# Kernel tuning notes

Hardware: AMD Instinct MI355X
Metric: run time of the kernel (lower is better)

Reference implementation:

```python
import jax, jax.numpy as jnp
import numpy as np

N_NODES = 32768
N_EDGES = 524288
IN_F = 256
OUT_F = 128
NB = 4


def setup_inputs() -> dict:
    key = jax.random.key(0)
    ks = jax.random.split(key, 12)
    s_in = 1.0 / np.sqrt(IN_F)
    s_out = 1.0 / np.sqrt(OUT_F)
    s_cat = 1.0 / np.sqrt(OUT_F * NB)
    return {
        "x": jax.random.normal(ks[0], (N_NODES, IN_F), dtype=jnp.float32),
        "edge_index": jax.random.randint(ks[1], (2, N_EDGES), 0, N_NODES, dtype=jnp.int64),
        "Wb": jax.random.uniform(ks[2], (NB, IN_F, OUT_F), jnp.float32, -s_in, s_in),
        "bb": jax.random.uniform(ks[3], (NB, OUT_F), jnp.float32, -s_in, s_in),
        "W1": jax.random.uniform(ks[4], (NB, OUT_F, OUT_F), jnp.float32, -s_out, s_out),
        "b1": jax.random.uniform(ks[5], (NB, OUT_F), jnp.float32, -s_out, s_out),
        "W2": jax.random.uniform(ks[6], (NB, OUT_F, OUT_F), jnp.float32, -s_out, s_out),
        "b2": jax.random.uniform(ks[7], (NB, OUT_F), jnp.float32, -s_out, s_out),
        "branch_gates": jnp.ones((NB,), dtype=jnp.float32),
        "temperature": jnp.asarray(1.0, dtype=jnp.float32),
        "Wo": jax.random.uniform(ks[8], (OUT_F * NB, OUT_F), jnp.float32, -s_cat, s_cat),
        "bo": jax.random.uniform(ks[9], (OUT_F,), jnp.float32, -s_cat, s_cat),
    }


def _scatter_mean_step(h, row, col, inv_deg):
    # gather per-edge source features, mean-reduce onto destination nodes
    sums = jax.ops.segment_sum(h[row], col, num_segments=N_NODES)
    return sums * inv_deg


def reference(x, edge_index, Wb, bb, W1, b1, W2, b2, branch_gates, temperature, Wo, bo):
    row, col = edge_index[0], edge_index[1]
    deg = jax.ops.segment_sum(jnp.ones((N_EDGES,), x.dtype), col, num_segments=N_NODES)
    inv_deg = (1.0 / jnp.maximum(deg, 1.0))[:, None]  # empty segments -> 0 (scatter_mean semantics)

    gates = jax.nn.softmax(branch_gates / temperature)

    branch_outputs = []
    for i in range(NB):
        h = x @ Wb[i] + bb[i]                   # [N, OUT_F]
        for _ in range(i):                       # scale = scales[i % 4] = i
            h = _scatter_mean_step(h, row, col, inv_deg)
        h = jax.nn.relu(h @ W1[i] + b1[i]) @ W2[i] + b2[i]
        branch_outputs.append(h * gates[i])

    concat = jnp.concatenate(branch_outputs, axis=1)  # [N, NB*OUT_F]
    return concat @ Wo + bo
```

## Files before the change

kernel.cpp:

```cpp
#include <hip/hip_runtime.h>
#include <math.h>

#define N_NODES 32768
#define N_EDGES 524288
#define IN_F    256
#define OUT_F   128
#define NB      4
#define STRIDE  96

#define NE_BLK   256
#define CONV_BLK 1024
#define GX_BLK   2048
#define GEMM_BLK (N_NODES / 128)
#define M_BLK    (N_NODES / 256)

typedef __attribute__((ext_vector_type(8))) short bf16x8;
typedef __attribute__((ext_vector_type(4))) float f32x4;
typedef __attribute__((ext_vector_type(4))) ushort u16x4;

__device__ __forceinline__ ushort f2b(float f) {
    uint u = __float_as_uint(f);
    return (ushort)((u + 0x7fffu + ((u >> 16) & 1u)) >> 16);
}
__device__ __forceinline__ float b2f_lo(uint v) { return __uint_as_float(v << 16); }
__device__ __forceinline__ float b2f_hi(uint v) { return __uint_as_float(v & 0xffff0000u); }

__device__ __forceinline__ float softmax_gate(const float* bg, const float* temp, int i) {
    float T = temp[0];
    float mx = fmaxf(fmaxf(bg[0], bg[1]), fmaxf(bg[2], bg[3]));
    float e0 = expf((bg[0] - mx) / T), e1 = expf((bg[1] - mx) / T);
    float e2 = expf((bg[2] - mx) / T), e3 = expf((bg[3] - mx) / T);
    float s = e0 + e1 + e2 + e3;
    float ei = (i == 0) ? e0 : (i == 1) ? e1 : (i == 2) ? e2 : e3;
    return ei / s;
}

__device__ __forceinline__ int detect_i32(const int* __restrict__ ei, int* sflag) {
    if (threadIdx.x < 64) {
        unsigned long long b = __ballot(ei[2 * threadIdx.x + 1] != 0);
        if (threadIdx.x == 0) *sflag = (b != 0ull) ? 1 : 0;
    }
    __syncthreads();
    return *sflag;
}

__global__ __launch_bounds__(256) void fill_all_kernel(
    const int* __restrict__ ei, int* __restrict__ cursor, int* __restrict__ srcs,
    const float* __restrict__ x, ushort* __restrict__ xb,
    const float* __restrict__ Wb, const float* __restrict__ W1,
    const float* __restrict__ W2, const float* __restrict__ Wo,
    const float* __restrict__ bb, const float* __restrict__ b2,
    const float* __restrict__ bo, const float* __restrict__ bg,
    const float* __restrict__ temp,
    ushort* __restrict__ WcT, ushort* __restrict__ WzT,
    float* __restrict__ u, float* __restrict__ cvec) {
    __shared__ float smem[16 * 128];
    __shared__ int sflag;
    int b = blockIdx.x;
    int tid = threadIdx.x;
    if (b < NE_BLK) {
        int i32 = detect_i32(ei, &sflag);
#pragma unroll
        for (int it = 0; it < 8; it++) {
            int e = b * 2048 + it * 256 + tid;
            int r, c;
            if (i32 == 0) {
                r = __builtin_nontemporal_load(ei + 2 * e);
                c = __builtin_nontemporal_load(ei + 2 * (N_EDGES + e));
            } else {
                r = __builtin_nontemporal_load(ei + e);
                c = __builtin_nontemporal_load(ei + N_EDGES + e);
            }
            int slot = atomicAdd(&cursor[c], 1);
            if (slot < STRIDE) srcs[(size_t)c * STRIDE + slot] = r;
        }
        return;
    }
    b -= NE_BLK;
    if (b < CONV_BLK) {
#pragma unroll
        for (int it = 0; it < 8; it++) {
            int idx = b * 2048 + it * 256 + tid;
            f32x4 v = __builtin_nontemporal_load((const f32x4*)x + idx);
            u16x4 o;
            o.x = f2b(v.x); o.y = f2b(v.y); o.z = f2b(v.z); o.w = f2b(v.w);
            *((u16x4*)xb + idx) = o;
        }
        return;
    }
    b -= CONV_BLK;
    int f = tid & 127, rh = tid >> 7;
    if (b < 64) {
        int i = b >> 4, k0 = (b & 15) * 16;
#pragma unroll
        for (int rr = 0; rr < 8; rr++)
            smem[(rh * 8 + rr) * 128 + f] = Wb[((size_t)i * IN_F + k0 + rh * 8 + rr) * OUT_F + f];
        __syncthreads();
        float acc[8] = {};
        const float* W1i = W1 + (size_t)i * OUT_F * OUT_F;
        for (int j = 0; j < OUT_F; j++) {
            float w1 = W1i[j * OUT_F + f];
#pragma unroll
            for (int rr = 0; rr < 8; rr++) acc[rr] += smem[(rh * 8 + rr) * 128 + j] * w1;
        }
        ushort tmp[8];
#pragma unroll
        for (int rr = 0; rr < 8; rr++) tmp[rr] = f2b(acc[rr]);
        *(uint4*)(WcT + ((size_t)i * OUT_F + f) * IN_F + k0 + rh * 8) = *(uint4*)tmp;
    } else if (b < 96) {
        int id = b - 64;
        int i = id >> 3, j0 = (id & 7) * 16;
#pragma unroll
        for (int rr = 0; rr < 8; rr++)
            smem[(rh * 8 + rr) * 128 + f] = W2[((size_t)i * OUT_F + j0 + rh * 8 + rr) * OUT_F + f];
        __syncthreads();
        float acc[8] = {};
        for (int l = 0; l < OUT_F; l++) {
            float wo = Wo[((size_t)i * OUT_F + l) * OUT_F + f];
#pragma unroll
            for (int rr = 0; rr < 8; rr++) acc[rr] += smem[(rh * 8 + rr) * 128 + l] * wo;
        }
        float g = softmax_gate(bg, temp, i);
        ushort tmp[8];
#pragma unroll
        for (int rr = 0; rr < 8; rr++) tmp[rr] = f2b(g * acc[rr]);
        *(uint4*)(WzT + (size_t)f * (NB * OUT_F) + i * OUT_F + j0 + rh * 8) = *(uint4*)tmp;
    } else {
        int id = b - 96;
        int jc = rh;
        if (id < NB) {
            int i = id;
            float partial = 0.f;
            for (int j = jc * 64; j < jc * 64 + 64; j++)
                partial += bb[i * OUT_F + j] * W1[((size_t)i * OUT_F + j) * OUT_F + f];
            smem[jc * 128 + f] = partial;
            __syncthreads();
            if (jc == 0) u[i * OUT_F + f] = smem[f] + smem[128 + f];
        } else {
            int i = id - NB;
            float partial = 0.f;
            for (int j = jc * 64; j < jc * 64 + 64; j++)
                partial += b2[i * OUT_F + j] * Wo[((size_t)i * OUT_F + j) * OUT_F + f];
            smem[jc * 128 + f] = partial;
            __syncthreads();
            if (jc == 0) {
                float tot = (smem[f] + smem[128 + f]) * softmax_gate(bg, temp, i);
                if (i == 0) tot += bo[f];
                atomicAdd(&cvec[f], tot);
            }
        }
    }
}

#define ACC8(A, V)                                                              \
    A[0] += b2f_lo(V.x); A[1] += b2f_hi(V.x);                                   \
    A[2] += b2f_lo(V.y); A[3] += b2f_hi(V.y);                                   \
    A[4] += b2f_lo(V.z); A[5] += b2f_hi(V.z);                                   \
    A[6] += b2f_lo(V.w); A[7] += b2f_hi(V.w)

#define GATHER_SLICE(INBUF, STRIDE_F)                                           \
    float a[8] = {0.f,0.f,0.f,0.f,0.f,0.f,0.f,0.f};                             \
    float b_[8] = {0.f,0.f,0.f,0.f,0.f,0.f,0.f,0.f};                            \
    int p = s;                                                                  \
    for (; p + 16 <= e; p += 16) {                                              \
        int2 ss = *(const int2*)(srcs + p + 2 * g);                             \
        uint4 v0 = *(const uint4*)(INBUF + (size_t)ss.x * STRIDE_F + colOff);   \
        uint4 v1 = *(const uint4*)(INBUF + (size_t)ss.y * STRIDE_F + colOff);   \
        ACC8(a, v0); ACC8(b_, v1);                                              \
    }                                                                           \
    for (; p + 8 <= e; p += 8) {                                                \
        int src = srcs[p + g];                                                  \
        uint4 v0 = *(const uint4*)(INBUF + (size_t)src * STRIDE_F + colOff);    \
        ACC8(a, v0);                                                            \
    }                                                                           \
    if (p + g < e) {                                                            \
        int src = srcs[p + g];                                                  \
        uint4 v0 = *(const uint4*)(INBUF + (size_t)src * STRIDE_F + colOff);    \
        ACC8(b_, v0);                                                           \
    }                                                                           \
    _Pragma("unroll") for (int k = 0; k < 8; k++) a[k] += b_[k];                \
    _Pragma("unroll") for (int k = 0; k < 8; k++) a[k] += __shfl_down(a[k], 32);\
    _Pragma("unroll") for (int k = 0; k < 8; k++) a[k] += __shfl_down(a[k], 16);\
    _Pragma("unroll") for (int k = 0; k < 8; k++) a[k] += __shfl_down(a[k], 8);

__global__ __launch_bounds__(256, 8) void prop_x_kernel(
    const ushort* __restrict__ xb, ushort* __restrict__ X1b,
    const int* __restrict__ deg, float* __restrict__ m2,
    const int* __restrict__ srcs) {
    int blk = blockIdx.x;
    int tid = threadIdx.x;
    if (blk < M_BLK) {
        int n = blk * 256 + tid;
        int d = deg[n];
        int s = n * STRIDE, e = s + ((d < STRIDE) ? d : STRIDE);
        float sum = 0.f;
        for (int p = s; p < e; ++p) sum += (deg[srcs[p]] > 0) ? 1.0f : 0.0f;
        m2[n] = sum / (float)((d > 1) ? d : 1);
        return;
    }
    blk -= M_BLK;
    int pass = blk >> 11, blk2 = blk & 2047;
    int lane = tid & 63;
    int g = lane >> 3, f8 = lane & 7;
    int colOff = pass * 64 + f8 * 8;
    for (int i = 0; i < 4; i++) {
        int node = blk2 * 16 + i * 4 + (tid >> 6);
        int d = deg[node];
        int s = node * STRIDE, e = s + ((d < STRIDE) ? d : STRIDE);
        GATHER_SLICE(xb, IN_F);
        if (lane < 8) {
            float w = 1.0f / (float)((d > 1) ? d : 1);
            uint4 o;
            o.x = (uint)f2b(a[0] * w) | ((uint)f2b(a[1] * w) << 16);
            o.y = (uint)f2b(a[2] * w) | ((uint)f2b(a[3] * w) << 16);
            o.z = (uint)f2b(a[4] * w) | ((uint)f2b(a[5] * w) << 16);
            o.w = (uint)f2b(a[6] * w) | ((uint)f2b(a[7] * w) << 16);
            *(uint4*)(X1b + (size_t)node * IN_F + colOff) = o;
        }
    }
}

__global__ __launch_bounds__(256) void gemmP_kernel(
    const ushort* __restrict__ xb, const ushort* __restrict__ X1b,
    const ushort* __restrict__ WcT, const float* __restrict__ u,
    const float* __restrict__ b1, const int* __restrict__ deg,
    ushort* __restrict__ R, ushort* __restrict__ PQ) {
    int y = blockIdx.y;
    const ushort* A = (y == 0) ? xb : X1b;
    const ushort* WT = WcT + (size_t)y * OUT_F * IN_F;
    int m0 = blockIdx.x * 128;
    __shared__ ushort As[128][72];
    __shared__ ushort Bs[128][72];
    int tid = threadIdx.x;
    int wv = tid >> 6, lane = tid & 63, quad = lane >> 4, lm = lane & 15;
    f32x4 acc[2][8];
    f32x4 zero = {0.f, 0.f, 0.f, 0.f};
#pragma unroll
    for (int i = 0; i < 2; i++)
#pragma unroll
        for (int j = 0; j < 8; j++) acc[i][j] = zero;
    for (int k0 = 0; k0 < IN_F; k0 += 64) {
        __syncthreads();
#pragma unroll
        for (int it = 0; it < 4; it++) {
            int c = tid + 256 * it;
            int r = c >> 3, c8 = c & 7;
            *(uint4*)&As[r][c8 * 8] = *(const uint4*)(A + (size_t)(m0 + r) * IN_F + k0 + c8 * 8);
            *(uint4*)&Bs[r][c8 * 8] = *(const uint4*)(WT + (size_t)r * IN_F + k0 + c8 * 8);
        }
        __syncthreads();
#pragma unroll
        for (int ks = 0; ks < 2; ks++) {
            bf16x8 af0 = *(const bf16x8*)&As[wv * 32 + lm][ks * 32 + quad * 8];
            bf16x8 af1 = *(const bf16x8*)&As[wv * 32 + 16 + lm][ks * 32 + quad * 8];
#pragma unroll
            for (int nt = 0; nt < 8; nt++) {
                bf16x8 bf = *(const bf16x8*)&Bs[nt * 16 + lm][ks * 32 + quad * 8];
                acc[0][nt] = __builtin_amdgcn_mfma_f32_16x16x32_bf16(af0, bf, acc[0][nt], 0, 0, 0);
                acc[1][nt] = __builtin_amdgcn_mfma_f32_16x16x32_bf16(af1, bf, acc[1][nt], 0, 0, 0);
            }
        }
    }
    if (y >= 2) {
        int pqoff = (y - 2) * OUT_F;
#pragma unroll
        for (int mt = 0; mt < 2; mt++)
#pragma unroll
            for (int r = 0; r < 4; r++) {
                int row = m0 + wv * 32 + mt * 16 + quad * 4 + r;
#pragma unroll
                for (int nt = 0; nt < 8; nt++) {
                    int col = nt * 16 + lm;
                    PQ[(size_t)row * IN_F + pqoff + col] = f2b(acc[mt][nt][r]);
                }
            }
    } else {
        float uv[8], bv[8];
#pragma unroll
        for (int nt = 0; nt < 8; nt++) {
            int col = nt * 16 + lm;
            uv[nt] = u[y * OUT_F + col];
            bv[nt] = b1[y * OUT_F + col];
        }
#pragma unroll
        for (int mt = 0; mt < 2; mt++)
#pragma unroll
            for (int r = 0; r < 4; r++) {
                int row = m0 + wv * 32 + mt * 16 + quad * 4 + r;
                float mval = (y == 0) ? 1.0f : ((deg[row] > 0) ? 1.0f : 0.0f);
#pragma unroll
                for (int nt = 0; nt < 8; nt++) {
                    int col = nt * 16 + lm;
                    float h = acc[mt][nt][r] + mval * uv[nt] + bv[nt];
                    R[(size_t)row * (NB * OUT_F) + y * OUT_F + col] = f2b(fmaxf(h, 0.f));
                }
            }
    }
}

__global__ __launch_bounds__(256, 8) void prop_pq_kernel(
    const ushort* __restrict__ PQ, ushort* __restrict__ R, ushort* __restrict__ Qp,
    const int* __restrict__ deg, const float* __restrict__ m2, float* __restrict__ m3,
    const float* __restrict__ u2, const float* __restrict__ b12,
    const int* __restrict__ srcs) {
    int blk = blockIdx.x;
    int tid = threadIdx.x;
    if (blk < M_BLK) {
        int n = blk * 256 + tid;
        int d = deg[n];
        int s = n * STRIDE, e = s + ((d < STRIDE) ? d : STRIDE);
        float sum = 0.f;
        for (int p = s; p < e; ++p) sum += m2[srcs[p]];
        m3[n] = sum / (float)((d > 1) ? d : 1);
        return;
    }
    blk -= M_BLK;
    int pass = blk >> 11, blk2 = blk & 2047;
    int lane = tid & 63;
    int g = lane >> 3, f8 = lane & 7;
    int colOff = pass * 64 + f8 * 8;
    for (int i = 0; i < 4; i++) {
        int node = blk2 * 16 + i * 4 + (tid >> 6);
        int d = deg[node];
        int s = node * STRIDE, e = s + ((d < STRIDE) ? d : STRIDE);
        GATHER_SLICE(PQ, IN_F);
        if (lane < 8) {
            float w = 1.0f / (float)((d > 1) ? d : 1);
            if (pass < 2) {
                int col = colOff;
                float mv = m2[node];
                float4 ua = *(const float4*)(u2 + col);
                float4 ub = *(const float4*)(u2 + col + 4);
                float4 ba = *(const float4*)(b12 + col);
                float4 bb2 = *(const float4*)(b12 + col + 4);
                float o_[8];
                o_[0] = fmaxf(a[0] * w + mv * ua.x + ba.x, 0.f);
                o_[1] = fmaxf(a[1] * w + mv * ua.y + ba.y, 0.f);
                o_[2] = fmaxf(a[2] * w + mv * ua.z + ba.z, 0.f);
                o_[3] = fmaxf(a[3] * w + mv * ua.w + ba.w, 0.f);
                o_[4] = fmaxf(a[4] * w + mv * ub.x + bb2.x, 0.f);
                o_[5] = fmaxf(a[5] * w + mv * ub.y + bb2.y, 0.f);
                o_[6] = fmaxf(a[6] * w + mv * ub.z + bb2.z, 0.f);
                o_[7] = fmaxf(a[7] * w + mv * ub.w + bb2.w, 0.f);
                uint4 o;
                o.x = (uint)f2b(o_[0]) | ((uint)f2b(o_[1]) << 16);
                o.y = (uint)f2b(o_[2]) | ((uint)f2b(o_[3]) << 16);
                o.z = (uint)f2b(o_[4]) | ((uint)f2b(o_[5]) << 16);
                o.w = (uint)f2b(o_[6]) | ((uint)f2b(o_[7]) << 16);
                *(uint4*)(R + (size_t)node * (NB * OUT_F) + 2 * OUT_F + col) = o;
            } else {
                int col = colOff - 128;
                uint4 o;
                o.x = (uint)f2b(a[0] * w) | ((uint)f2b(a[1] * w) << 16);
                o.y = (uint)f2b(a[2] * w) | ((uint)f2b(a[3] * w) << 16);
                o.z = (uint)f2b(a[4] * w) | ((uint)f2b(a[5] * w) << 16);
                o.w = (uint)f2b(a[6] * w) | ((uint)f2b(a[7] * w) << 16);
                *(uint4*)(Qp + (size_t)node * OUT_F + col) = o;
            }
        }
    }
}

__global__ __launch_bounds__(256, 8) void prop_q_kernel(
    const ushort* __restrict__ Qp, ushort* __restrict__ R,
    const int* __restrict__ deg, const float* __restrict__ m3,
    const float* __restrict__ u3, const float* __restrict__ b13,
    const int* __restrict__ srcs) {
    int blk = blockIdx.x;
    int tid = threadIdx.x;
    int pass = blk >> 11, blk2 = blk & 2047;
    int lane = tid & 63;
    int g = lane >> 3, f8 = lane & 7;
    int colOff = pass * 64 + f8 * 8;
    for (int i = 0; i < 4; i++) {
        int node = blk2 * 16 + i * 4 + (tid >> 6);
        int d = deg[node];
        int s = node * STRIDE, e = s + ((d < STRIDE) ? d : STRIDE);
        GATHER_SLICE(Qp, OUT_F);
        if (lane < 8) {
            float w = 1.0f / (float)((d > 1) ? d : 1);
            float mv = m3[node];
            int col = colOff;
            float4 ua = *(const float4*)(u3 + col);
            float4 ub = *(const float4*)(u3 + col + 4);
            float4 ba = *(const float4*)(b13 + col);
            float4 bb2 = *(const float4*)(b13 + col + 4);
            float o_[8];
            o_[0] = fmaxf(a[0] * w + mv * ua.x + ba.x, 0.f);
            o_[1] = fmaxf(a[1] * w + mv * ua.y + ba.y, 0.f);
            o_[2] = fmaxf(a[2] * w + mv * ua.z + ba.z, 0.f);
            o_[3] = fmaxf(a[3] * w + mv * ua.w + ba.w, 0.f);
            o_[4] = fmaxf(a[4] * w + mv * ub.x + bb2.x, 0.f);
            o_[5] = fmaxf(a[5] * w + mv * ub.y + bb2.y, 0.f);
            o_[6] = fmaxf(a[6] * w + mv * ub.z + bb2.z, 0.f);
            o_[7] = fmaxf(a[7] * w + mv * ub.w + bb2.w, 0.f);
            uint4 o;
            o.x = (uint)f2b(o_[0]) | ((uint)f2b(o_[1]) << 16);
            o.y = (uint)f2b(o_[2]) | ((uint)f2b(o_[3]) << 16);
            o.z = (uint)f2b(o_[4]) | ((uint)f2b(o_[5]) << 16);
            o.w = (uint)f2b(o_[6]) | ((uint)f2b(o_[7]) << 16);
            *(uint4*)(R + (size_t)node * (NB * OUT_F) + 3 * OUT_F + col) = o;
        }
    }
}

__global__ __launch_bounds__(256) void gemm2_mfma_kernel(
    const ushort* __restrict__ R, const ushort* __restrict__ WzT,
    const float* __restrict__ cvec, float* __restrict__ out) {
    int m0 = blockIdx.x * 128;
    const int K = NB * OUT_F;
    __shared__ ushort As[128][72];
    __shared__ ushort Bs[128][72];
    int tid = threadIdx.x;
    int wv = tid >> 6, lane = tid & 63, quad = lane >> 4, lm = lane & 15;
    f32x4 acc[2][8];
    f32x4 zero = {0.f, 0.f, 0.f, 0.f};
#pragma unroll
    for (int i = 0; i < 2; i++)
#pragma unroll
        for (int j = 0; j < 8; j++) acc[i][j] = zero;
    for (int k0 = 0; k0 < K; k0 += 64) {
        __syncthreads();
#pragma unroll
        for (int it = 0; it < 4; it++) {
            int c = tid + 256 * it;
            int r = c >> 3, c8 = c & 7;
            *(uint4*)&As[r][c8 * 8] = *(const uint4*)(R + (size_t)(m0 + r) * K + k0 + c8 * 8);
            *(uint4*)&Bs[r][c8 * 8] = *(const uint4*)(WzT + (size_t)r * K + k0 + c8 * 8);
        }
        __syncthreads();
#pragma unroll
        for (int ks = 0; ks < 2; ks++) {
            bf16x8 af0 = *(const bf16x8*)&As[wv * 32 + lm][ks * 32 + quad * 8];
            bf16x8 af1 = *(const bf16x8*)&As[wv * 32 + 16 + lm][ks * 32 + quad * 8];
#pragma unroll
            for (int nt = 0; nt < 8; nt++) {
                bf16x8 bf = *(const bf16x8*)&Bs[nt * 16 + lm][ks * 32 + quad * 8];
                acc[0][nt] = __builtin_amdgcn_mfma_f32_16x16x32_bf16(af0, bf, acc[0][nt], 0, 0, 0);
                acc[1][nt] = __builtin_amdgcn_mfma_f32_16x16x32_bf16(af1, bf, acc[1][nt], 0, 0, 0);
            }
        }
    }
    float cb[8];
#pragma unroll
    for (int nt = 0; nt < 8; nt++) cb[nt] = cvec[nt * 16 + lm];
#pragma unroll
    for (int mt = 0; mt < 2; mt++)
#pragma unroll
        for (int r = 0; r < 4; r++) {
            int row = m0 + wv * 32 + mt * 16 + quad * 4 + r;
#pragma unroll
            for (int nt = 0; nt < 8; nt++) {
                int col = nt * 16 + lm;
                __builtin_nontemporal_store(acc[mt][nt][r] + cb[nt],
                                            out + (size_t)row * OUT_F + col);
            }
        }
}

extern "C" void kernel_launch(void* const* d_in, const int* in_sizes, int n_in,
                              void* d_out, int out_size, void* d_ws, size_t ws_size,
                              hipStream_t stream) {
    const float* x    = (const float*)d_in[0];
    const int*   ei   = (const int*)d_in[1];
    const float* Wb   = (const float*)d_in[2];
    const float* bb   = (const float*)d_in[3];
    const float* W1   = (const float*)d_in[4];
    const float* b1   = (const float*)d_in[5];
    const float* W2   = (const float*)d_in[6];
    const float* b2   = (const float*)d_in[7];
    const float* bg   = (const float*)d_in[8];
    const float* temp = (const float*)d_in[9];
    const float* Wo   = (const float*)d_in[10];
    const float* bo   = (const float*)d_in[11];
    float* out = (float*)d_out;

    char* w = (char*)d_ws;
    size_t used = 0;
    auto alloc = [&](size_t bytes) {
        char* p = w + used;
        used += (bytes + 255) & ~(size_t)255;
        return p;
    };
    int*    cursor = (int*)alloc(N_NODES * 4);
    float*  cvec   = (float*)alloc(OUT_F * 4);
    int*    srcs   = (int*)alloc((size_t)N_NODES * STRIDE * 4);
    float*  m2v    = (float*)alloc(N_NODES * 4);
    float*  m3v    = (float*)alloc(N_NODES * 4);
    float*  u      = (float*)alloc(NB * OUT_F * 4);
    ushort* WcT    = (ushort*)alloc((size_t)NB * IN_F * OUT_F * 2);
    ushort* WzT    = (ushort*)alloc((size_t)NB * OUT_F * OUT_F * 2);
    ushort* xb     = (ushort*)alloc((size_t)N_NODES * IN_F * 2);
    ushort* X1b    = (ushort*)alloc((size_t)N_NODES * IN_F * 2);
    ushort* PQ     = (ushort*)alloc((size_t)N_NODES * IN_F * 2);
    ushort* Qp     = (ushort*)alloc((size_t)N_NODES * OUT_F * 2);
    ushort* R      = (ushort*)alloc((size_t)N_NODES * NB * OUT_F * 2);
    if (used > ws_size) return;

    int* deg = cursor;

    hipMemsetAsync(cursor, 0, N_NODES * 4 + 512, stream);

    fill_all_kernel<<<NE_BLK + CONV_BLK + 104, 256, 0, stream>>>(
        ei, cursor, srcs, x, xb, Wb, W1, W2, Wo, bb, b2, bo, bg, temp, WcT, WzT, u, cvec);

    prop_x_kernel<<<M_BLK + 4 * GX_BLK, 256, 0, stream>>>(xb, X1b, deg, m2v, srcs);

    {
        dim3 grid(GEMM_BLK, 4);
        gemmP_kernel<<<grid, 256, 0, stream>>>(xb, X1b, WcT, u, b1, deg, R, PQ);
    }

    prop_pq_kernel<<<M_BLK + 4 * GX_BLK, 256, 0, stream>>>(
        PQ, R, Qp, deg, m2v, m3v, u + 2 * OUT_F, b1 + 2 * OUT_F, srcs);

    prop_q_kernel<<<2 * GX_BLK, 256, 0, stream>>>(
        Qp, R, deg, m3v, u + 3 * OUT_F, b1 + 3 * OUT_F, srcs);

    gemm2_mfma_kernel<<<GEMM_BLK, 256, 0, stream>>>(R, WzT, cvec, out);
}
```

Before: 288.6 us.

## Store neighbor lists as 16-bit indices and widen gather slices per wave

Neighbor source indices are now stored as ushort, which halves the CSR-like buffer written in the fill kernel and read in every gather. The gather mapping also changes from 8 edge groups × 8 lanes × 16 bytes to 2 halves × 32 lanes × 8 bytes. Each wave now covers 128 columns per pass, so half as many passes and blocks are launched and the shuffle reduction shrinks to a single step. The trade-off is smaller per-lane loads and fewer edges processed in parallel per wave, which may lower memory-level parallelism. Node ids fit in 16 bits only because N_NODES is 32768.

After: 261.5 us, median of 2. 9.4% less time.

```diff
diff --git a/kernel.cpp b/kernel.cpp
--- a/kernel.cpp
+++ b/kernel.cpp
@@ -45,7 +45,7 @@
 }
 
 __global__ __launch_bounds__(256) void fill_all_kernel(
-    const int* __restrict__ ei, int* __restrict__ cursor, int* __restrict__ srcs,
+    const int* __restrict__ ei, int* __restrict__ cursor, ushort* __restrict__ srcs,
     const float* __restrict__ x, ushort* __restrict__ xb,
     const float* __restrict__ Wb, const float* __restrict__ W1,
     const float* __restrict__ W2, const float* __restrict__ Wo,
@@ -72,7 +72,7 @@
                 c = __builtin_nontemporal_load(ei + N_EDGES + e);
             }
             int slot = atomicAdd(&cursor[c], 1);
-            if (slot < STRIDE) srcs[(size_t)c * STRIDE + slot] = r;
+            if (slot < STRIDE) srcs[(size_t)c * STRIDE + slot] = (ushort)r;
         }
         return;
     }
@@ -152,41 +152,50 @@
     }
 }
 
-#define ACC8(A, V)                                                              \
+#define ACC4(A, V)                                                              \
     A[0] += b2f_lo(V.x); A[1] += b2f_hi(V.x);                                   \
-    A[2] += b2f_lo(V.y); A[3] += b2f_hi(V.y);                                   \
-    A[4] += b2f_lo(V.z); A[5] += b2f_hi(V.z);                                   \
-    A[6] += b2f_lo(V.w); A[7] += b2f_hi(V.w)
-
-#define GATHER_SLICE(INBUF, STRIDE_F)                                           \
-    float a[8] = {0.f,0.f,0.f,0.f,0.f,0.f,0.f,0.f};                             \
-    float b_[8] = {0.f,0.f,0.f,0.f,0.f,0.f,0.f,0.f};                            \
+    A[2] += b2f_lo(V.y); A[3] += b2f_hi(V.y)
+
+#define GATHER_SLICE(INBUF, ROWSTRIDE)                                          \
+    float a0[4] = {0.f,0.f,0.f,0.f};                                            \
+    float a1[4] = {0.f,0.f,0.f,0.f};                                            \
     int p = s;                                                                  \
-    for (; p + 16 <= e; p += 16) {                                              \
-        int2 ss = *(const int2*)(srcs + p + 2 * g);                             \
-        uint4 v0 = *(const uint4*)(INBUF + (size_t)ss.x * STRIDE_F + colOff);   \
-        uint4 v1 = *(const uint4*)(INBUF + (size_t)ss.y * STRIDE_F + colOff);   \
-        ACC8(a, v0); ACC8(b_, v1);                                              \
+    for (; p + 12 <= e; p += 12) {                                              \
+        int base = p + 6 * half;                                                \
+        uint s01 = *(const uint*)(srcs + base);                                 \
+        uint s23 = *(const uint*)(srcs + base + 2);                             \
+        uint s45 = *(const uint*)(srcs + base + 4);                             \
+        uint2 v0 = *(const uint2*)(INBUF + (size_t)(s01 & 0xffffu) * ROWSTRIDE + colOff); \
+        uint2 v1 = *(const uint2*)(INBUF + (size_t)(s01 >> 16)    * ROWSTRIDE + colOff); \
+        uint2 v2 = *(const uint2*)(INBUF + (size_t)(s23 & 0xffffu) * ROWSTRIDE + colOff); \
+        uint2 v3 = *(const uint2*)(INBUF + (size_t)(s23 >> 16)    * ROWSTRIDE + colOff); \
+        uint2 v4 = *(const uint2*)(INBUF + (size_t)(s45 & 0xffffu) * ROWSTRIDE + colOff); \
+        uint2 v5 = *(const uint2*)(INBUF + (size_t)(s45 >> 16)    * ROWSTRIDE + colOff); \
+        ACC4(a0, v0); ACC4(a1, v1); ACC4(a0, v2);                               \
+        ACC4(a1, v3); ACC4(a0, v4); ACC4(a1, v5);                               \
     }                                                                           \
-    for (; p + 8 <= e; p += 8) {                                                \
-        int src = srcs[p + g];                                                  \
-        uint4 v0 = *(const uint4*)(INBUF + (size_t)src * STRIDE_F + colOff);    \
-        ACC8(a, v0);                                                            \
+    for (; p + 4 <= e; p += 4) {                                                \
+        uint ss = *(const uint*)(srcs + p + 2 * half);                          \
+        uint2 v0 = *(const uint2*)(INBUF + (size_t)(ss & 0xffffu) * ROWSTRIDE + colOff); \
+        uint2 v1 = *(const uint2*)(INBUF + (size_t)(ss >> 16)    * ROWSTRIDE + colOff); \
+        ACC4(a0, v0); ACC4(a1, v1);                                             \
     }                                                                           \
-    if (p + g < e) {                                                            \
-        int src = srcs[p + g];                                                  \
-        uint4 v0 = *(const uint4*)(INBUF + (size_t)src * STRIDE_F + colOff);    \
-        ACC8(b_, v0);                                                           \
+    for (; p + half < e; p += 2) {                                              \
+        int src = srcs[p + half];                                               \
+        uint2 v0 = *(const uint2*)(INBUF + (size_t)src * ROWSTRIDE + colOff);   \
+        ACC4(a0, v0);                                                           \
     }                                                                           \
-    _Pragma("unroll") for (int k = 0; k < 8; k++) a[k] += b_[k];                \
-    _Pragma("unroll") for (int k = 0; k < 8; k++) a[k] += __shfl_down(a[k], 32);\
-    _Pragma("unroll") for (int k = 0; k < 8; k++) a[k] += __shfl_down(a[k], 16);\
-    _Pragma("unroll") for (int k = 0; k < 8; k++) a[k] += __shfl_down(a[k], 8);
+    _Pragma("unroll") for (int k = 0; k < 4; k++) a0[k] += a1[k];               \
+    _Pragma("unroll") for (int k = 0; k < 4; k++) a0[k] += __shfl_down(a0[k], 32);
+
+#define PACK2(A, W)                                                             \
+    { o.x = (uint)f2b(A[0] * W) | ((uint)f2b(A[1] * W) << 16);                  \
+      o.y = (uint)f2b(A[2] * W) | ((uint)f2b(A[3] * W) << 16); }
 
 __global__ __launch_bounds__(256, 8) void prop_x_kernel(
     const ushort* __restrict__ xb, ushort* __restrict__ X1b,
     const int* __restrict__ deg, float* __restrict__ m2,
-    const int* __restrict__ srcs) {
+    const ushort* __restrict__ srcs) {
     int blk = blockIdx.x;
     int tid = threadIdx.x;
     if (blk < M_BLK) {
@@ -201,21 +210,18 @@
     blk -= M_BLK;
     int pass = blk >> 11, blk2 = blk & 2047;
     int lane = tid & 63;
-    int g = lane >> 3, f8 = lane & 7;
-    int colOff = pass * 64 + f8 * 8;
+    int half = lane >> 5, fl = lane & 31;
+    int colOff = pass * 128 + fl * 4;
     for (int i = 0; i < 4; i++) {
         int node = blk2 * 16 + i * 4 + (tid >> 6);
         int d = deg[node];
         int s = node * STRIDE, e = s + ((d < STRIDE) ? d : STRIDE);
         GATHER_SLICE(xb, IN_F);
-        if (lane < 8) {
+        if (half == 0) {
             float w = 1.0f / (float)((d > 1) ? d : 1);
-            uint4 o;
-            o.x = (uint)f2b(a[0] * w) | ((uint)f2b(a[1] * w) << 16);
-            o.y = (uint)f2b(a[2] * w) | ((uint)f2b(a[3] * w) << 16);
-            o.z = (uint)f2b(a[4] * w) | ((uint)f2b(a[5] * w) << 16);
-            o.w = (uint)f2b(a[6] * w) | ((uint)f2b(a[7] * w) << 16);
-            *(uint4*)(X1b + (size_t)node * IN_F + colOff) = o;
+            uint2 o;
+            PACK2(a0, w);
+            *(uint2*)(X1b + (size_t)node * IN_F + colOff) = o;
         }
     }
 }
@@ -302,7 +308,7 @@
     const ushort* __restrict__ PQ, ushort* __restrict__ R, ushort* __restrict__ Qp,
     const int* __restrict__ deg, const float* __restrict__ m2, float* __restrict__ m3,
     const float* __restrict__ u2, const float* __restrict__ b12,
-    const int* __restrict__ srcs) {
+    const ushort* __restrict__ srcs) {
     int blk = blockIdx.x;
     int tid = threadIdx.x;
     if (blk < M_BLK) {
@@ -317,45 +323,34 @@
     blk -= M_BLK;
     int pass = blk >> 11, blk2 = blk & 2047;
     int lane = tid & 63;
-    int g = lane >> 3, f8 = lane & 7;
-    int colOff = pass * 64 + f8 * 8;
+    int half = lane >> 5, fl = lane & 31;
+    int colOff = pass * 128 + fl * 4;
     for (int i = 0; i < 4; i++) {
         int node = blk2 * 16 + i * 4 + (tid >> 6);
         int d = deg[node];
         int s = node * STRIDE, e = s + ((d < STRIDE) ? d : STRIDE);
         GATHER_SLICE(PQ, IN_F);
-        if (lane < 8) {
+        if (half == 0) {
             float w = 1.0f / (float)((d > 1) ? d : 1);
-            if (pass < 2) {
-                int col = colOff;
+            if (pass == 0) {
+                int col = fl * 4;
                 float mv = m2[node];
                 float4 ua = *(const float4*)(u2 + col);
-                float4 ub = *(const float4*)(u2 + col + 4);
                 float4 ba = *(const float4*)(b12 + col);
-                float4 bb2 = *(const float4*)(b12 + col + 4);
-                float o_[8];
-                o_[0] = fmaxf(a[0] * w + mv * ua.x + ba.x, 0.f);
-                o_[1] = fmaxf(a[1] * w + mv * ua.y + ba.y, 0.f);
-                o_[2] = fmaxf(a[2] * w + mv * ua.z + ba.z, 0.f);
-                o_[3] = fmaxf(a[3] * w + mv * ua.w + ba.w, 0.f);
-                o_[4] = fmaxf(a[4] * w + mv * ub.x + bb2.x, 0.f);
-                o_[5] = fmaxf(a[5] * w + mv * ub.y + bb2.y, 0.f);
-                o_[6] = fmaxf(a[6] * w + mv * ub.z + bb2.z, 0.f);
-                o_[7] = fmaxf(a[7] * w + mv * ub.w + bb2.w, 0.f);
-                uint4 o;
+                float o_[4];
+                o_[0] = fmaxf(a0[0] * w + mv * ua.x + ba.x, 0.f);
+                o_[1] = fmaxf(a0[1] * w + mv * ua.y + ba.y, 0.f);
+                o_[2] = fmaxf(a0[2] * w + mv * ua.z + ba.z, 0.f);
+                o_[3] = fmaxf(a0[3] * w + mv * ua.w + ba.w, 0.f);
+                uint2 o;
                 o.x = (uint)f2b(o_[0]) | ((uint)f2b(o_[1]) << 16);
                 o.y = (uint)f2b(o_[2]) | ((uint)f2b(o_[3]) << 16);
-                o.z = (uint)f2b(o_[4]) | ((uint)f2b(o_[5]) << 16);
-                o.w = (uint)f2b(o_[6]) | ((uint)f2b(o_[7]) << 16);
-                *(uint4*)(R + (size_t)node * (NB * OUT_F) + 2 * OUT_F + col) = o;
+                *(uint2*)(R + (size_t)node * (NB * OUT_F) + 2 * OUT_F + col) = o;
             } else {
-                int col = colOff - 128;
-                uint4 o;
-                o.x = (uint)f2b(a[0] * w) | ((uint)f2b(a[1] * w) << 16);
-                o.y = (uint)f2b(a[2] * w) | ((uint)f2b(a[3] * w) << 16);
-                o.z = (uint)f2b(a[4] * w) | ((uint)f2b(a[5] * w) << 16);
-                o.w = (uint)f2b(a[6] * w) | ((uint)f2b(a[7] * w) << 16);
-                *(uint4*)(Qp + (size_t)node * OUT_F + col) = o;
+                int col = fl * 4;
+                uint2 o;
+                PACK2(a0, w);
+                *(uint2*)(Qp + (size_t)node * OUT_F + col) = o;
             }
         }
     }
@@ -365,41 +360,31 @@
     const ushort* __restrict__ Qp, ushort* __restrict__ R,
     const int* __restrict__ deg, const float* __restrict__ m3,
     const float* __restrict__ u3, const float* __restrict__ b13,
-    const int* __restrict__ srcs) {
-    int blk = blockIdx.x;
+    const ushort* __restrict__ srcs) {
     int tid = threadIdx.x;
-    int pass = blk >> 11, blk2 = blk & 2047;
     int lane = tid & 63;
-    int g = lane >> 3, f8 = lane & 7;
-    int colOff = pass * 64 + f8 * 8;
+    int half = lane >> 5, fl = lane & 31;
+    int colOff = fl * 4;
     for (int i = 0; i < 4; i++) {
-        int node = blk2 * 16 + i * 4 + (tid >> 6);
+        int node = blockIdx.x * 16 + i * 4 + (tid >> 6);
         int d = deg[node];
         int s = node * STRIDE, e = s + ((d < STRIDE) ? d : STRIDE);
         GATHER_SLICE(Qp, OUT_F);
-        if (lane < 8) {
+        if (half == 0) {
             float w = 1.0f / (float)((d > 1) ? d : 1);
             float mv = m3[node];
-            int col = colOff;
+            int col = fl * 4;
             float4 ua = *(const float4*)(u3 + col);
-            float4 ub = *(const float4*)(u3 + col + 4);
             float4 ba = *(const float4*)(b13 + col);
-            float4 bb2 = *(const float4*)(b13 + col + 4);
-            float o_[8];
-            o_[0] = fmaxf(a[0] * w + mv * ua.x + ba.x, 0.f);
-            o_[1] = fmaxf(a[1] * w + mv * ua.y + ba.y, 0.f);
-            o_[2] = fmaxf(a[2] * w + mv * ua.z + ba.z, 0.f);
-            o_[3] = fmaxf(a[3] * w + mv * ua.w + ba.w, 0.f);
-            o_[4] = fmaxf(a[4] * w + mv * ub.x + bb2.x, 0.f);
-            o_[5] = fmaxf(a[5] * w + mv * ub.y + bb2.y, 0.f);
-            o_[6] = fmaxf(a[6] * w + mv * ub.z + bb2.z, 0.f);
-            o_[7] = fmaxf(a[7] * w + mv * ub.w + bb2.w, 0.f);
-            uint4 o;
+            float o_[4];
+            o_[0] = fmaxf(a0[0] * w + mv * ua.x + ba.x, 0.f);
+            o_[1] = fmaxf(a0[1] * w + mv * ua.y + ba.y, 0.f);
+            o_[2] = fmaxf(a0[2] * w + mv * ua.z + ba.z, 0.f);
+            o_[3] = fmaxf(a0[3] * w + mv * ua.w + ba.w, 0.f);
+            uint2 o;
             o.x = (uint)f2b(o_[0]) | ((uint)f2b(o_[1]) << 16);
             o.y = (uint)f2b(o_[2]) | ((uint)f2b(o_[3]) << 16);
-            o.z = (uint)f2b(o_[4]) | ((uint)f2b(o_[5]) << 16);
-            o.w = (uint)f2b(o_[6]) | ((uint)f2b(o_[7]) << 16);
-            *(uint4*)(R + (size_t)node * (NB * OUT_F) + 3 * OUT_F + col) = o;
+            *(uint2*)(R + (size_t)node * (NB * OUT_F) + 3 * OUT_F + col) = o;
         }
     }
 }
@@ -484,7 +469,7 @@
     };
     int*    cursor = (int*)alloc(N_NODES * 4);
     float*  cvec   = (float*)alloc(OUT_F * 4);
-    int*    srcs   = (int*)alloc((size_t)N_NODES * STRIDE * 4);
+    ushort* srcs   = (ushort*)alloc((size_t)N_NODES * STRIDE * 2);
     float*  m2v    = (float*)alloc(N_NODES * 4);
     float*  m3v    = (float*)alloc(N_NODES * 4);
     float*  u      = (float*)alloc(NB * OUT_F * 4);
@@ -504,17 +489,17 @@
     fill_all_kernel<<<NE_BLK + CONV_BLK + 104, 256, 0, stream>>>(
         ei, cursor, srcs, x, xb, Wb, W1, W2, Wo, bb, b2, bo, bg, temp, WcT, WzT, u, cvec);
 
-    prop_x_kernel<<<M_BLK + 4 * GX_BLK, 256, 0, stream>>>(xb, X1b, deg, m2v, srcs);
+    prop_x_kernel<<<M_BLK + 2 * GX_BLK, 256, 0, stream>>>(xb, X1b, deg, m2v, srcs);
 
     {
         dim3 grid(GEMM_BLK, 4);
         gemmP_kernel<<<grid, 256, 0, stream>>>(xb, X1b, WcT, u, b1, deg, R, PQ);
     }
 
-    prop_pq_kernel<<<M_BLK + 4 * GX_BLK, 256, 0, stream>>>(
+    prop_pq_kernel<<<M_BLK + 2 * GX_BLK, 256, 0, stream>>>(
         PQ, R, Qp, deg, m2v, m3v, u + 2 * OUT_F, b1 + 2 * OUT_F, srcs);
 
-    prop_q_kernel<<<2 * GX_BLK, 256, 0, stream>>>(
+    prop_q_kernel<<<GX_BLK, 256, 0, stream>>>(
         Qp, R, deg, m3v, u + 3 * OUT_F, b1 + 3 * OUT_F, srcs);
 
     gemm2_mfma_kernel<<<GEMM_BLK, 256, 0, stream>>>(R, WzT, cvec, out);
```
